# Optimization experiments

Measured on AMD Instinct MI355X. Metric: run time of the kernel, lower is better.

Reference implementation:

```python
import jax, jax.numpy as jnp
import numpy as np

B, S, D, L = 32, 1024, 768, 12

def setup_inputs() -> dict:
    key = jax.random.key(0)
    ks = jax.random.split(key, 10)
    hidden_states = jax.random.normal(ks[0], (B, S, D), dtype=jnp.float32)
    Wq = jax.random.normal(ks[1], (L, D, D), dtype=jnp.float32) * 0.02
    Wk = jax.random.normal(ks[2], (L, D, D), dtype=jnp.float32) * 0.02
    Wv = jax.random.normal(ks[3], (L, D, D), dtype=jnp.float32) * 0.02
    bq = jnp.zeros((L, D), dtype=jnp.float32)
    bk = jnp.zeros((L, D), dtype=jnp.float32)
    bv = jnp.zeros((L, D), dtype=jnp.float32)
    l_k = jnp.full((L, D), 0.8, dtype=jnp.float32)  # iA3 scales, init 0.8 per source
    l_v = jnp.full((L, D), 0.8, dtype=jnp.float32)
    W_head = jax.random.normal(ks[4], (D, 1), dtype=jnp.float32) * 0.02
    b_head = jnp.zeros((1,), dtype=jnp.float32)
    return {"hidden_states": hidden_states, "Wq": Wq, "bq": bq, "Wk": Wk, "bk": bk,
            "Wv": Wv, "bv": bv, "l_k": l_k, "l_v": l_v, "W_head": W_head, "b_head": b_head}

def reference(hidden_states, Wq, bq, Wk, bk, Wv, bv, l_k, l_v, W_head, b_head):
    scale = 1.0 / jnp.sqrt(jnp.float32(D))

    def layer_step(h, params):
        wq, bq_i, wk, bk_i, wv, bv_i, lk, lv = params
        Q = jnp.einsum('bsd,de->bse', h, wq) + bq_i
        K = (jnp.einsum('bsd,de->bse', h, wk) + bk_i) * lk  # iA3 per-channel scale on K
        V = (jnp.einsum('bsd,de->bse', h, wv) + bv_i) * lv  # iA3 per-channel scale on V
        attn = jax.nn.softmax(jnp.einsum('bqd,bkd->bqk', Q, K) * scale, axis=-1)
        h_new = jnp.einsum('bqk,bkd->bqd', attn, V)  # note: no residual/LN, matches source
        return h_new, None

    h, _ = jax.lax.scan(layer_step, hidden_states, (Wq, bq, Wk, bk, Wv, bv, l_k, l_v))
    pooled = h[:, 0, :]  # CLS token
    out = pooled @ W_head + b_head  # [B, 1]
    return out[:, 0]
```

## Files before the change

kernel.cpp:

```cpp
#include <hip/hip_runtime.h>
#include <hip/hip_fp16.h>
#include <math.h>

#define B_ 32
#define S_ 1024
#define D_ 768
#define L_ 12
#define SD 786432LL
#define SS 1048576LL
#define DD 589824LL
#define LDL 1769472LL

typedef _Float16 half8 __attribute__((ext_vector_type(8)));
typedef float f32x4 __attribute__((ext_vector_type(4)));
typedef unsigned short u16;

#define SW(lr) ((((lr) ^ ((lr) >> 3)) & 7))

__global__ __launch_bounds__(256, 2)
void gemm_qkv_k(const __half* __restrict__ A, const __half* __restrict__ Wt,
                const float* __restrict__ biasC, const float* __restrict__ scaleC,
                float aBias,
                __half* __restrict__ CQ, __half* __restrict__ CK, __half* __restrict__ CVt,
                int nBase, int tilesX, int mPerXcd)
{
    __shared__ __align__(16) u16 smem[16384];
    const int K = 768;

    const int flat = blockIdx.x;
    const int xcd = flat & 7;
    const int jj = flat >> 3;
    const int mLocal = jj / tilesX;
    const int nxI = jj - mLocal * tilesX;
    const int n0 = nxI * 128;
    const int m0 = (xcd * mPerXcd + mLocal) * 128;

    const int t = threadIdx.x;
    const int l = t & 63, w = t >> 6;
    const int wm = (w & 1) * 64, wn = (w >> 1) * 64;

    const int u0 = t, u1 = t + 256;
    const int r0 = u0 >> 2, c0 = (u0 & 3) ^ (r0 & 3);
    const int r1 = u1 >> 2, c1 = (u1 & 3) ^ (r1 & 3);
    const __half* gA0 = A + (long long)(m0 + r0) * K + c0 * 8;
    const __half* gA1 = A + (long long)(m0 + r1) * K + c1 * 8;
    const __half* gB0 = Wt + (long long)(n0 + r0) * K + c0 * 8;
    const __half* gB1 = Wt + (long long)(n0 + r1) * K + c1 * 8;
    u16* lA0 = &smem[u0 * 8];
    u16* lA1 = &smem[u1 * 8];
    u16* lB0 = &smem[4096 + u0 * 8];
    u16* lB1 = &smem[4096 + u1 * 8];

    int aoff[4], boff[4];
    const int kc = l >> 4;
    #pragma unroll
    for (int mt = 0; mt < 4; ++mt) {
        int rr = wm + mt * 16 + (l & 15);
        aoff[mt] = (rr * 4 + (kc ^ (rr & 3))) * 8;
        int rb = wn + mt * 16 + (l & 15);
        boff[mt] = (rb * 4 + (kc ^ (rb & 3))) * 8;
    }

    f32x4 acc[4][4];
    #pragma unroll
    for (int i = 0; i < 4; ++i)
        #pragma unroll
        for (int j = 0; j < 4; ++j)
            acc[i][j] = (f32x4){0.f, 0.f, 0.f, 0.f};

    for (int k0 = 0; k0 < K; k0 += 32) {
        __builtin_amdgcn_global_load_lds((const __attribute__((address_space(1))) void*)(gA0 + k0),
                                         (__attribute__((address_space(3))) void*)lA0, 16, 0, 0);
        __builtin_amdgcn_global_load_lds((const __attribute__((address_space(1))) void*)(gA1 + k0),
                                         (__attribute__((address_space(3))) void*)lA1, 16, 0, 0);
        __builtin_amdgcn_global_load_lds((const __attribute__((address_space(1))) void*)(gB0 + k0),
                                         (__attribute__((address_space(3))) void*)lB0, 16, 0, 0);
        __builtin_amdgcn_global_load_lds((const __attribute__((address_space(1))) void*)(gB1 + k0),
                                         (__attribute__((address_space(3))) void*)lB1, 16, 0, 0);
        __syncthreads();

        half8 af[4], bf[4];
        #pragma unroll
        for (int mt = 0; mt < 4; ++mt) af[mt] = *(const half8*)(const void*)&smem[aoff[mt]];
        #pragma unroll
        for (int nt = 0; nt < 4; ++nt) bf[nt] = *(const half8*)(const void*)&smem[4096 + boff[nt]];

        #pragma unroll
        for (int nt = 0; nt < 4; ++nt)
            #pragma unroll
            for (int mt = 0; mt < 4; ++mt)
                acc[mt][nt] = __builtin_amdgcn_mfma_f32_16x16x32_f16(af[mt], bf[nt], acc[mt][nt], 0, 0, 0);
        __syncthreads();
    }

    const int nCat0 = n0 + nBase;
    const int region = nCat0 / 768;
    const int colBase = nCat0 - region * 768;

    float badd[4], bmul[4];
    #pragma unroll
    for (int nt = 0; nt < 4; ++nt) {
        int gn = nCat0 + wn + nt * 16 + (l & 15);
        badd[nt] = aBias * biasC[gn];
        bmul[nt] = scaleC[gn];
    }

    const int qbase = w * 4096;
    #pragma unroll
    for (int mt = 0; mt < 4; ++mt) {
        #pragma unroll
        for (int nt = 0; nt < 4; ++nt) {
            #pragma unroll
            for (int i = 0; i < 4; ++i) {
                int lrow = mt * 16 + ((l >> 4) << 2) + i;
                int lcol = nt * 16 + (l & 15);
                float v = (acc[mt][nt][i] + badd[nt]) * bmul[nt];
                int cc = lcol >> 3, c7 = lcol & 7;
                smem[qbase + lrow * 64 + ((cc ^ SW(lrow)) << 3) + c7] =
                    __half_as_ushort(__float2half(v));
            }
        }
    }
    __syncthreads();

    if (region < 2) {
        __half* Creg = region ? CK : CQ;
        #pragma unroll
        for (int p = 0; p < 8; ++p) {
            int u = t + p * 256;
            int R = u >> 4, cc = u & 15;
            int qb = ((R >> 6) + ((cc >> 3) << 1)) * 4096;
            int lr = R & 63, lcc = cc & 7;
            half8 val = *(const half8*)(const void*)&smem[qb + lr * 64 + ((lcc ^ SW(lr)) << 3)];
            *(half8*)(void*)&Creg[(long long)(m0 + R) * 768 + colBase + cc * 8] = val;
        }
    } else {
        #pragma unroll
        for (int p = 0; p < 8; ++p) {
            int u = t + p * 256;
            int Crow = u >> 4, mcc = u & 15;
            __align__(16) u16 tmp[8];
            #pragma unroll
            for (int j = 0; j < 8; ++j) {
                int m = mcc * 8 + j;
                int qb = ((m >> 6) + ((Crow >> 6) << 1)) * 4096;
                int lr = m & 63, lcol = Crow & 63;
                int lcc = lcol >> 3;
                tmp[j] = smem[qb + lr * 64 + ((lcc ^ SW(lr)) << 3) + (lcol & 7)];
            }
            long long b = m0 >> 10;
            __half* dst = CVt + b * SD + (long long)(colBase + Crow) * 1024 + (m0 & 1023) + mcc * 8;
            *(half8*)(void*)dst = *(const half8*)(const void*)tmp;
        }
    }
}

template<int SWIZ, int MODE>
__global__ __launch_bounds__(256, 2)
void gemm_att_k(const __half* __restrict__ A, const __half* __restrict__ B,
                float aAcc, __half* __restrict__ C, int K, int ldc,
                long long sA, long long sB, long long sC,
                int tilesX, int tilesPB, int bpx,
                float* __restrict__ rsp, const float* __restrict__ invsum)
{
    __shared__ __align__(16) u16 smem[16384];
    __shared__ float sums[128 * 17];

    int nxI, ny;
    long long bz;
    if (SWIZ) {
        int flat = blockIdx.x;
        int xcd = flat & 7;
        int j = flat >> 3;
        int bLocal = j / tilesPB;
        int tt = j - bLocal * tilesPB;
        bz = (long long)(xcd * bpx + bLocal);
        ny = tt / tilesX;
        nxI = tt - ny * tilesX;
    } else {
        nxI = blockIdx.x; ny = blockIdx.y; bz = blockIdx.z;
    }

    const int t = threadIdx.x;
    const int l = t & 63, w = t >> 6;
    const int n0 = nxI * 128;
    const int m0 = ny * 128;
    A += bz * sA; B += bz * sB; C += bz * sC;

    const int wm = (w & 1) * 64, wn = (w >> 1) * 64;

    const int u0 = t, u1 = t + 256;
    const int r0 = u0 >> 2, c0 = (u0 & 3) ^ (r0 & 3);
    const int r1 = u1 >> 2, c1 = (u1 & 3) ^ (r1 & 3);
    const __half* gA0 = A + (long long)(m0 + r0) * K + c0 * 8;
    const __half* gA1 = A + (long long)(m0 + r1) * K + c1 * 8;
    const __half* gB0 = B + (long long)(n0 + r0) * K + c0 * 8;
    const __half* gB1 = B + (long long)(n0 + r1) * K + c1 * 8;
    u16* lA0 = &smem[u0 * 8];
    u16* lA1 = &smem[u1 * 8];
    u16* lB0 = &smem[4096 + u0 * 8];
    u16* lB1 = &smem[4096 + u1 * 8];

    int aoff[4], boff[4];
    const int kc = l >> 4;
    #pragma unroll
    for (int mt = 0; mt < 4; ++mt) {
        int rr = wm + mt * 16 + (l & 15);
        aoff[mt] = (rr * 4 + (kc ^ (rr & 3))) * 8;
        int rb = wn + mt * 16 + (l & 15);
        boff[mt] = (rb * 4 + (kc ^ (rb & 3))) * 8;
    }

    f32x4 acc[4][4];
    #pragma unroll
    for (int i = 0; i < 4; ++i)
        #pragma unroll
        for (int j = 0; j < 4; ++j)
            acc[i][j] = (f32x4){0.f, 0.f, 0.f, 0.f};

    for (int k0 = 0; k0 < K; k0 += 32) {
        __builtin_amdgcn_global_load_lds((const __attribute__((address_space(1))) void*)(gA0 + k0),
                                         (__attribute__((address_space(3))) void*)lA0, 16, 0, 0);
        __builtin_amdgcn_global_load_lds((const __attribute__((address_space(1))) void*)(gA1 + k0),
                                         (__attribute__((address_space(3))) void*)lA1, 16, 0, 0);
        __builtin_amdgcn_global_load_lds((const __attribute__((address_space(1))) void*)(gB0 + k0),
                                         (__attribute__((address_space(3))) void*)lB0, 16, 0, 0);
        __builtin_amdgcn_global_load_lds((const __attribute__((address_space(1))) void*)(gB1 + k0),
                                         (__attribute__((address_space(3))) void*)lB1, 16, 0, 0);
        __syncthreads();

        half8 af[4], bf[4];
        #pragma unroll
        for (int mt = 0; mt < 4; ++mt) af[mt] = *(const half8*)(const void*)&smem[aoff[mt]];
        #pragma unroll
        for (int nt = 0; nt < 4; ++nt) bf[nt] = *(const half8*)(const void*)&smem[4096 + boff[nt]];

        #pragma unroll
        for (int nt = 0; nt < 4; ++nt)
            #pragma unroll
            for (int mt = 0; mt < 4; ++mt)
                acc[mt][nt] = __builtin_amdgcn_mfma_f32_16x16x32_f16(af[mt], bf[nt], acc[mt][nt], 0, 0, 0);
        __syncthreads();
    }

    float invr[4][4];
    if (MODE == 2) {
        #pragma unroll
        for (int mt = 0; mt < 4; ++mt)
            #pragma unroll
            for (int i = 0; i < 4; ++i)
                invr[mt][i] = invsum[bz * 1024 + m0 + wm + mt * 16 + ((l >> 4) << 2) + i];
    }

    const int qbase = w * 4096;
    #pragma unroll
    for (int mt = 0; mt < 4; ++mt) {
        #pragma unroll
        for (int nt = 0; nt < 4; ++nt) {
            #pragma unroll
            for (int i = 0; i < 4; ++i) {
                int lrow = mt * 16 + ((l >> 4) << 2) + i;
                int lcol = nt * 16 + (l & 15);
                float v;
                if (MODE == 1)      v = __expf(acc[mt][nt][i] * aAcc);
                else                v = acc[mt][nt][i] * aAcc * invr[mt][i];
                int cc = lcol >> 3, c7 = lcol & 7;
                smem[qbase + lrow * 64 + ((cc ^ SW(lrow)) << 3) + c7] =
                    __half_as_ushort(__float2half(v));
            }
        }
    }
    __syncthreads();

    #pragma unroll
    for (int p = 0; p < 8; ++p) {
        int u = t + p * 256;
        int R = u >> 4, cc = u & 15;
        int qb = ((R >> 6) + ((cc >> 3) << 1)) * 4096;
        int lr = R & 63, lcc = cc & 7;
        half8 val = *(const half8*)(const void*)&smem[qb + lr * 64 + ((lcc ^ SW(lr)) << 3)];
        *(half8*)(void*)&C[(long long)(m0 + R) * ldc + n0 + cc * 8] = val;
        if (MODE == 1) {
            float s8 = 0.f;
            #pragma unroll
            for (int j = 0; j < 8; ++j) s8 += (float)val[j];
            sums[R * 17 + cc] = s8;
        }
    }
    if (MODE == 1) {
        __syncthreads();
        if (t < 128) {
            float s = 0.f;
            #pragma unroll
            for (int c = 0; c < 16; ++c) s += sums[t * 17 + c];
            rsp[bz * 8192 + (long long)(m0 + t) * 8 + nxI] = s;
        }
    }
}

__global__ __launch_bounds__(256)
void rowsuminv_k(const float* __restrict__ rsp, float* __restrict__ inv, int n)
{
    int i = blockIdx.x * 256 + threadIdx.x;
    if (i < n) {
        const float* p = rsp + (long long)i * 8;
        float s = ((p[0] + p[1]) + (p[2] + p[3])) + ((p[4] + p[5]) + (p[6] + p[7]));
        inv[i] = 1.0f / s;
    }
}

__global__ __launch_bounds__(256)
void cvt32to16_k(const float* __restrict__ X, __half* __restrict__ Y)
{
    long long i = ((long long)blockIdx.x * 256 + threadIdx.x) * 4;
    float4 v = *(const float4*)&X[i];
    *(__half2*)&Y[i]     = __floats2half2_rn(v.x, v.y);
    *(__half2*)&Y[i + 2] = __floats2half2_rn(v.z, v.w);
}

__global__ __launch_bounds__(256)
void wtrans_k(const float* __restrict__ W, __half* __restrict__ Wt,
              long long ldL, int rowOff)
{
    __shared__ float Ls[64][65];
    const int lyr = blockIdx.z;
    const int k0 = blockIdx.y * 64, n0 = blockIdx.x * 64;
    const float* src = W + (long long)lyr * DD;
    __half* dst = Wt + (long long)lyr * ldL;
    const int t = threadIdx.x;
    #pragma unroll
    for (int p = 0; p < 4; ++p) {
        int u = t + p * 256;
        int r = u >> 4, c4 = (u & 15) * 4;
        float4 v = *(const float4*)&src[(long long)(k0 + r) * D_ + n0 + c4];
        Ls[r][c4] = v.x; Ls[r][c4 + 1] = v.y; Ls[r][c4 + 2] = v.z; Ls[r][c4 + 3] = v.w;
    }
    __syncthreads();
    #pragma unroll
    for (int p = 0; p < 2; ++p) {
        int u = t + p * 256;
        int n = u >> 3, kc8 = (u & 7) * 8;
        __align__(16) u16 tmp[8];
        #pragma unroll
        for (int j = 0; j < 8; ++j) {
            _Float16 h = (_Float16)Ls[kc8 + j][n];
            tmp[j] = *(const u16*)&h;
        }
        *(half8*)(void*)&dst[(long long)(rowOff + n0 + n) * D_ + k0 + kc8] =
            *(const half8*)(const void*)tmp;
    }
}

__global__ __launch_bounds__(256)
void bscat_k(const float* __restrict__ bq, const float* __restrict__ bk,
             const float* __restrict__ bv, const float* __restrict__ lk,
             const float* __restrict__ lv, float* __restrict__ bsb,
             float* __restrict__ bss)
{
    int i = blockIdx.x * 256 + threadIdx.x;
    if (i >= L_ * 2304) return;
    int l = i / 2304, p = i - l * 2304;
    int r = p / 768, c = p - r * 768;
    float b, s;
    if (r == 0)      { b = bq[l * 768 + c]; s = 1.f; }
    else if (r == 1) { b = bk[l * 768 + c]; s = lk[l * 768 + c]; }
    else             { b = bv[l * 768 + c]; s = lv[l * 768 + c]; }
    bsb[i] = b; bss[i] = s;
}

__global__ __launch_bounds__(256)
void q0_k(const __half* __restrict__ H16, const __half* __restrict__ Wcat,
          const float* __restrict__ bq, float* __restrict__ q0f, float sig)
{
    const int b = blockIdx.x;
    const int n = blockIdx.y * 256 + threadIdx.x;
    const int t = threadIdx.x;
    __shared__ __half hrow[768];
    const __half* h = H16 + (long long)b * SD;
    hrow[t] = h[t]; hrow[t + 256] = h[t + 256]; hrow[t + 512] = h[t + 512];
    __syncthreads();
    const __half* wr = Wcat + 11LL * LDL + (long long)n * 768;
    float acc = 0.f;
    for (int k = 0; k < 768; ++k) acc += (float)hrow[k] * (float)wr[k];
    q0f[b * 768 + n] = acc + sig * bq[11 * 768 + n];
}

__global__ __launch_bounds__(256)
void s0_k(const float* __restrict__ q0f, const __half* __restrict__ K16,
          float* __restrict__ s0f, int b0, float aQK)
{
    const int z = blockIdx.x;
    const int b = b0 + z;
    const int s = blockIdx.y * 256 + threadIdx.x;
    const int t = threadIdx.x;
    __shared__ float qrow[768];
    qrow[t] = q0f[b * 768 + t];
    qrow[t + 256] = q0f[b * 768 + t + 256];
    qrow[t + 512] = q0f[b * 768 + t + 512];
    __syncthreads();
    const __half* kr = K16 + (long long)z * SD + (long long)s * 768;
    float acc = 0.f;
    for (int k = 0; k < 768; ++k) acc += qrow[k] * (float)kr[k];
    s0f[b * 1024 + s] = acc * aQK;
}

__global__ __launch_bounds__(256)
void sm0_k(float* __restrict__ s0f, int b0)
{
    float* p = s0f + (long long)(b0 + blockIdx.x) * 1024;
    const int t = threadIdx.x;
    float v[4];
    float mx = -1e30f;
    #pragma unroll
    for (int j = 0; j < 4; ++j) { v[j] = p[t + 256 * j]; mx = fmaxf(mx, v[j]); }
    __shared__ float red[256];
    red[t] = mx; __syncthreads();
    for (int s = 128; s > 0; s >>= 1) { if (t < s) red[t] = fmaxf(red[t], red[t + s]); __syncthreads(); }
    mx = red[0];
    __syncthreads();
    float sum = 0.f;
    #pragma unroll
    for (int j = 0; j < 4; ++j) { v[j] = __expf(v[j] - mx); sum += v[j]; }
    red[t] = sum; __syncthreads();
    for (int s = 128; s > 0; s >>= 1) { if (t < s) red[t] += red[t + s]; __syncthreads(); }
    const float inv = 1.0f / red[0];
    __syncthreads();
    #pragma unroll
    for (int j = 0; j < 4; ++j) p[t + 256 * j] = v[j] * inv;
}

__global__ __launch_bounds__(256)
void o0_k(const float* __restrict__ p0f, const __half* __restrict__ Vt16,
          float* __restrict__ o0f, int b0, float invSig)
{
    const int z = blockIdx.x;
    const int b = b0 + z;
    const int d = blockIdx.y * 256 + threadIdx.x;
    const int t = threadIdx.x;
    __shared__ float prow[1024];
    #pragma unroll
    for (int j = 0; j < 4; ++j) prow[t + 256 * j] = p0f[b * 1024 + t + 256 * j];
    __syncthreads();
    const __half* vr = Vt16 + (long long)z * SD + (long long)d * 1024;
    float acc = 0.f;
    for (int s = 0; s < 1024; ++s) acc += prow[s] * (float)vr[s];
    o0f[b * 768 + d] = acc * invSig;
}

__global__ __launch_bounds__(256)
void headf_k(const float* __restrict__ o0f, const float* __restrict__ Wh,
             const float* __restrict__ bh, float* __restrict__ out)
{
    const int b = blockIdx.x;
    const int t = threadIdx.x;
    float s = 0.f;
    for (int d = t; d < 768; d += 256) s += o0f[b * 768 + d] * Wh[d];
    __shared__ float red[256];
    red[t] = s; __syncthreads();
    for (int k = 128; k > 0; k >>= 1) { if (t < k) red[t] += red[t + k]; __syncthreads(); }
    if (t == 0) out[b] = red[0] + bh[0];
}

extern "C" void kernel_launch(void* const* d_in, const int* in_sizes, int n_in,
                              void* d_out, int out_size, void* d_ws, size_t ws_size,
                              hipStream_t stream)
{
    const float* hs = (const float*)d_in[0];
    const float* Wq = (const float*)d_in[1];
    const float* bq = (const float*)d_in[2];
    const float* Wk = (const float*)d_in[3];
    const float* bk = (const float*)d_in[4];
    const float* Wv = (const float*)d_in[5];
    const float* bv = (const float*)d_in[6];
    const float* lk = (const float*)d_in[7];
    const float* lv = (const float*)d_in[8];
    const float* Wh = (const float*)d_in[9];
    const float* bh = (const float*)d_in[10];
    float* outp = (float*)d_out;

    __half* H16  = (__half*)d_ws;
    __half* Wcat = H16 + (long long)B_ * SD;
    float*  bsb  = (float*)(Wcat + 12LL * LDL);
    float*  bss  = bsb + 12 * 2304;
    float*  q0f  = bss + 12 * 2304;
    float*  s0f  = q0f + 32 * 768;
    float*  o0f  = s0f + 32 * 1024;
    float*  rsp  = o0f + 32 * 768;
    float*  inv  = rsp + 32LL * 8192;
    __half* Q16  = (__half*)(inv + 32 * 1024);

    const size_t baseBytes = (size_t)((char*)Q16 - (char*)d_ws);
    const size_t perG = ((size_t)(3 * SD) + (size_t)SS) * 2;
    long long avail = (long long)ws_size - (long long)baseBytes;
    int G = (avail > 0) ? (int)(avail / perG) : 1;
    if (G >= 32) G = 32; else if (G >= 16) G = 16; else if (G >= 8) G = 8;
    if (G < 1) G = 1;
    __half* K16  = Q16 + (long long)G * SD;
    __half* Vt16 = K16 + (long long)G * SD;
    __half* P16  = Vt16 + (long long)G * SD;

    cvt32to16_k<<<dim3((int)((B_ * SD) / 1024)), 256, 0, stream>>>(hs, H16);
    wtrans_k<<<dim3(12, 12, 12), 256, 0, stream>>>(Wq, Wcat, LDL, 0);
    wtrans_k<<<dim3(12, 12, 12), 256, 0, stream>>>(Wk, Wcat, LDL, 768);
    wtrans_k<<<dim3(12, 12, 12), 256, 0, stream>>>(Wv, Wcat, LDL, 1536);
    bscat_k<<<dim3((L_ * 2304 + 255) / 256), 256, 0, stream>>>(bq, bk, bv, lk, lv, bsb, bss);

    const float scq = 0.036084391824351615f;
    float sig = 1.f;

    for (int lyr = 0; lyr < L_ - 1; ++lyr) {
        const __half* W = Wcat + (long long)lyr * LDL;
        const float* bb = bsb + lyr * 2304;
        const float* ss = bss + lyr * 2304;
        const float aQK = scq / (sig * sig);

        for (int b0 = 0; b0 < B_; b0 += G) {
            const int nb = (B_ - b0 < G) ? (B_ - b0) : G;
            const __half* hg = H16 + (long long)b0 * SD;

            gemm_qkv_k<<<dim3(18 * 8 * nb), 256, 0, stream>>>(
                hg, W, bb, ss, sig, Q16, K16, Vt16, 0, 18, nb);

            if ((nb & 7) == 0) {
                gemm_att_k<1, 1><<<dim3(nb * 64), 256, 0, stream>>>(
                    Q16, K16, aQK, P16, 768, 1024, SD, SD, SS, 8, 64, nb >> 3, rsp, nullptr);
            } else {
                gemm_att_k<0, 1><<<dim3(8, 8, nb), 256, 0, stream>>>(
                    Q16, K16, aQK, P16, 768, 1024, SD, SD, SS, 8, 64, 1, rsp, nullptr);
            }

            rowsuminv_k<<<dim3(nb * 4), 256, 0, stream>>>(rsp, inv, nb * 1024);

            if ((nb & 7) == 0) {
                gemm_att_k<1, 2><<<dim3(nb * 48), 256, 0, stream>>>(
                    P16, Vt16, 4.f, H16 + (long long)b0 * SD, 1024, 768, SS, SD, SD,
                    6, 48, nb >> 3, nullptr, inv);
            } else {
                gemm_att_k<0, 2><<<dim3(6, 8, nb), 256, 0, stream>>>(
                    P16, Vt16, 4.f, H16 + (long long)b0 * SD, 1024, 768, SS, SD, SD,
                    6, 48, 1, nullptr, inv);
            }
        }
        sig *= 4.f;
    }

    const float aQK = scq / (sig * sig);
    q0_k<<<dim3(B_, 3), 256, 0, stream>>>(H16, Wcat, bq, q0f, sig);

    for (int b0 = 0; b0 < B_; b0 += G) {
        const int nb = (B_ - b0 < G) ? (B_ - b0) : G;
        const __half* hg = H16 + (long long)b0 * SD;

        gemm_qkv_k<<<dim3(12 * 8 * nb), 256, 0, stream>>>(
            hg, Wcat + 11LL * LDL + 768LL * 768, bsb + 11 * 2304, bss + 11 * 2304,
            sig, K16 , K16, Vt16, 768, 12, nb);

        s0_k<<<dim3(nb, 4), 256, 0, stream>>>(q0f, K16, s0f, b0, aQK);
        sm0_k<<<dim3(nb), 256, 0, stream>>>(s0f, b0);
        o0_k<<<dim3(nb, 3), 256, 0, stream>>>(s0f, Vt16, o0f, b0, 1.f / sig);
    }

    headf_k<<<dim3(B_), 256, 0, stream>>>(o0f, Wh, bh, outp);
}
```

Baseline: 3.572 ms.

## Swap MFMA operands for packed epilogue stores and fuse row-sum inverse

Swaps the A/B operands of the MFMA so each lane holds four consecutive columns of one row. The epilogue can then convert them to half2 pairs and write 8-byte packed LDS stores under a new XOR swizzle, replacing per-element 2-byte stores. It also removes the separate rowsuminv kernel: the PV GEMM now sums the 8 partial row sums itself and divides once per row. Each PV block redoes the partial-sum reduction, which costs a few extra global loads in exchange for one fewer launch per batch group.

```diff
diff --git a/kernel.cpp b/kernel.cpp
--- a/kernel.cpp
+++ b/kernel.cpp
@@ -15,7 +15,6 @@
 typedef float f32x4 __attribute__((ext_vector_type(4)));
 typedef unsigned short u16;
 
-#define SW(lr) ((((lr) ^ ((lr) >> 3)) & 7))
 
 __global__ __launch_bounds__(256, 2)
 void gemm_qkv_k(const __half* __restrict__ A, const __half* __restrict__ Wt,
@@ -37,6 +36,7 @@
 
     const int t = threadIdx.x;
     const int l = t & 63, w = t >> 6;
+    const int quad = l >> 4;
     const int wm = (w & 1) * 64, wn = (w >> 1) * 64;
 
     const int u0 = t, u1 = t + 256;
@@ -89,7 +89,7 @@
         for (int nt = 0; nt < 4; ++nt)
             #pragma unroll
             for (int mt = 0; mt < 4; ++mt)
-                acc[mt][nt] = __builtin_amdgcn_mfma_f32_16x16x32_f16(af[mt], bf[nt], acc[mt][nt], 0, 0, 0);
+                acc[mt][nt] = __builtin_amdgcn_mfma_f32_16x16x32_f16(bf[nt], af[mt], acc[mt][nt], 0, 0, 0);
         __syncthreads();
     }
 
@@ -97,28 +97,30 @@
     const int region = nCat0 / 768;
     const int colBase = nCat0 - region * 768;
 
-    float badd[4], bmul[4];
+    const int qbase = w * 4096;
     #pragma unroll
     for (int nt = 0; nt < 4; ++nt) {
-        int gn = nCat0 + wn + nt * 16 + (l & 15);
-        badd[nt] = aBias * biasC[gn];
-        bmul[nt] = scaleC[gn];
-    }
-
-    const int qbase = w * 4096;
-    #pragma unroll
-    for (int mt = 0; mt < 4; ++mt) {
-        #pragma unroll
-        for (int nt = 0; nt < 4; ++nt) {
-            #pragma unroll
-            for (int i = 0; i < 4; ++i) {
-                int lrow = mt * 16 + ((l >> 4) << 2) + i;
-                int lcol = nt * 16 + (l & 15);
-                float v = (acc[mt][nt][i] + badd[nt]) * bmul[nt];
-                int cc = lcol >> 3, c7 = lcol & 7;
-                smem[qbase + lrow * 64 + ((cc ^ SW(lrow)) << 3) + c7] =
-                    __half_as_ushort(__float2half(v));
-            }
+        float badd[4], bmul[4];
+        #pragma unroll
+        for (int i = 0; i < 4; ++i) {
+            int gn = nCat0 + wn + nt * 16 + quad * 4 + i;
+            badd[i] = aBias * biasC[gn];
+            bmul[i] = scaleC[gn];
+        }
+        #pragma unroll
+        for (int mt = 0; mt < 4; ++mt) {
+            int lr = mt * 16 + (l & 15);
+            float v0 = (acc[mt][nt][0] + badd[0]) * bmul[0];
+            float v1 = (acc[mt][nt][1] + badd[1]) * bmul[1];
+            float v2 = (acc[mt][nt][2] + badd[2]) * bmul[2];
+            float v3 = (acc[mt][nt][3] + badd[3]) * bmul[3];
+            __half2 h01 = __floats2half2_rn(v0, v1);
+            __half2 h23 = __floats2half2_rn(v2, v3);
+            uint2 pk;
+            pk.x = *(const unsigned int*)&h01;
+            pk.y = *(const unsigned int*)&h23;
+            int pos = qbase + lr * 64 + (((nt ^ (lr & 3))) << 4) + (quad << 2);
+            *(uint2*)(void*)&smem[pos] = pk;
         }
     }
     __syncthreads();
@@ -130,8 +132,9 @@
             int u = t + p * 256;
             int R = u >> 4, cc = u & 15;
             int qb = ((R >> 6) + ((cc >> 3) << 1)) * 4096;
-            int lr = R & 63, lcc = cc & 7;
-            half8 val = *(const half8*)(const void*)&smem[qb + lr * 64 + ((lcc ^ SW(lr)) << 3)];
+            int lr = R & 63, hc = cc & 7;
+            int pos = qb + lr * 64 + (((hc >> 1) ^ (lr & 3)) << 4) + ((hc & 1) << 3);
+            half8 val = *(const half8*)(const void*)&smem[pos];
             *(half8*)(void*)&Creg[(long long)(m0 + R) * 768 + colBase + cc * 8] = val;
         }
     } else {
@@ -140,13 +143,14 @@
             int u = t + p * 256;
             int Crow = u >> 4, mcc = u & 15;
             __align__(16) u16 tmp[8];
+            int lc = Crow & 63;
             #pragma unroll
             for (int j = 0; j < 8; ++j) {
                 int m = mcc * 8 + j;
                 int qb = ((m >> 6) + ((Crow >> 6) << 1)) * 4096;
-                int lr = m & 63, lcol = Crow & 63;
-                int lcc = lcol >> 3;
-                tmp[j] = smem[qb + lr * 64 + ((lcc ^ SW(lr)) << 3) + (lcol & 7)];
+                int lr = m & 63;
+                int pos = qb + lr * 64 + (((lc >> 4) ^ (lr & 3)) << 4) + (lc & 15);
+                tmp[j] = smem[pos];
             }
             long long b = m0 >> 10;
             __half* dst = CVt + b * SD + (long long)(colBase + Crow) * 1024 + (m0 & 1023) + mcc * 8;
@@ -160,8 +164,7 @@
 void gemm_att_k(const __half* __restrict__ A, const __half* __restrict__ B,
                 float aAcc, __half* __restrict__ C, int K, int ldc,
                 long long sA, long long sB, long long sC,
-                int tilesX, int tilesPB, int bpx,
-                float* __restrict__ rsp, const float* __restrict__ invsum)
+                int tilesX, int tilesPB, int bpx, float* __restrict__ rsp)
 {
     __shared__ __align__(16) u16 smem[16384];
     __shared__ float sums[128 * 17];
@@ -183,6 +186,7 @@
 
     const int t = threadIdx.x;
     const int l = t & 63, w = t >> 6;
+    const int quad = l >> 4;
     const int n0 = nxI * 128;
     const int m0 = ny * 128;
     A += bz * sA; B += bz * sB; C += bz * sC;
@@ -239,35 +243,41 @@
         for (int nt = 0; nt < 4; ++nt)
             #pragma unroll
             for (int mt = 0; mt < 4; ++mt)
-                acc[mt][nt] = __builtin_amdgcn_mfma_f32_16x16x32_f16(af[mt], bf[nt], acc[mt][nt], 0, 0, 0);
+                acc[mt][nt] = __builtin_amdgcn_mfma_f32_16x16x32_f16(bf[nt], af[mt], acc[mt][nt], 0, 0, 0);
         __syncthreads();
     }
 
-    float invr[4][4];
-    if (MODE == 2) {
-        #pragma unroll
-        for (int mt = 0; mt < 4; ++mt)
-            #pragma unroll
-            for (int i = 0; i < 4; ++i)
-                invr[mt][i] = invsum[bz * 1024 + m0 + wm + mt * 16 + ((l >> 4) << 2) + i];
-    }
-
     const int qbase = w * 4096;
     #pragma unroll
     for (int mt = 0; mt < 4; ++mt) {
+        int lr = mt * 16 + (l & 15);
+        float scl = aAcc;
+        if (MODE == 2) {
+            const float* pr = rsp + bz * 8192 + (long long)(m0 + wm + lr) * 8;
+            float s = ((pr[0] + pr[1]) + (pr[2] + pr[3])) + ((pr[4] + pr[5]) + (pr[6] + pr[7]));
+            scl = aAcc / s;
+        }
         #pragma unroll
         for (int nt = 0; nt < 4; ++nt) {
-            #pragma unroll
-            for (int i = 0; i < 4; ++i) {
-                int lrow = mt * 16 + ((l >> 4) << 2) + i;
-                int lcol = nt * 16 + (l & 15);
-                float v;
-                if (MODE == 1)      v = __expf(acc[mt][nt][i] * aAcc);
-                else                v = acc[mt][nt][i] * aAcc * invr[mt][i];
-                int cc = lcol >> 3, c7 = lcol & 7;
-                smem[qbase + lrow * 64 + ((cc ^ SW(lrow)) << 3) + c7] =
-                    __half_as_ushort(__float2half(v));
+            float v0, v1, v2, v3;
+            if (MODE == 1) {
+                v0 = __expf(acc[mt][nt][0] * aAcc);
+                v1 = __expf(acc[mt][nt][1] * aAcc);
+                v2 = __expf(acc[mt][nt][2] * aAcc);
+                v3 = __expf(acc[mt][nt][3] * aAcc);
+            } else {
+                v0 = acc[mt][nt][0] * scl;
+                v1 = acc[mt][nt][1] * scl;
+                v2 = acc[mt][nt][2] * scl;
+                v3 = acc[mt][nt][3] * scl;
             }
+            __half2 h01 = __floats2half2_rn(v0, v1);
+            __half2 h23 = __floats2half2_rn(v2, v3);
+            uint2 pk;
+            pk.x = *(const unsigned int*)&h01;
+            pk.y = *(const unsigned int*)&h23;
+            int pos = qbase + lr * 64 + (((nt ^ (lr & 3))) << 4) + (quad << 2);
+            *(uint2*)(void*)&smem[pos] = pk;
         }
     }
     __syncthreads();
@@ -277,8 +287,9 @@
         int u = t + p * 256;
         int R = u >> 4, cc = u & 15;
         int qb = ((R >> 6) + ((cc >> 3) << 1)) * 4096;
-        int lr = R & 63, lcc = cc & 7;
-        half8 val = *(const half8*)(const void*)&smem[qb + lr * 64 + ((lcc ^ SW(lr)) << 3)];
+        int lr = R & 63, hc = cc & 7;
+        int pos = qb + lr * 64 + (((hc >> 1) ^ (lr & 3)) << 4) + ((hc & 1) << 3);
+        half8 val = *(const half8*)(const void*)&smem[pos];
         *(half8*)(void*)&C[(long long)(m0 + R) * ldc + n0 + cc * 8] = val;
         if (MODE == 1) {
             float s8 = 0.f;
@@ -295,17 +306,6 @@
             for (int c = 0; c < 16; ++c) s += sums[t * 17 + c];
             rsp[bz * 8192 + (long long)(m0 + t) * 8 + nxI] = s;
         }
-    }
-}
-
-__global__ __launch_bounds__(256)
-void rowsuminv_k(const float* __restrict__ rsp, float* __restrict__ inv, int n)
-{
-    int i = blockIdx.x * 256 + threadIdx.x;
-    if (i < n) {
-        const float* p = rsp + (long long)i * 8;
-        float s = ((p[0] + p[1]) + (p[2] + p[3])) + ((p[4] + p[5]) + (p[6] + p[7]));
-        inv[i] = 1.0f / s;
     }
 }
 
@@ -486,8 +486,7 @@
     float*  s0f  = q0f + 32 * 768;
     float*  o0f  = s0f + 32 * 1024;
     float*  rsp  = o0f + 32 * 768;
-    float*  inv  = rsp + 32LL * 8192;
-    __half* Q16  = (__half*)(inv + 32 * 1024);
+    __half* Q16  = (__half*)(rsp + 32LL * 8192);
 
     const size_t baseBytes = (size_t)((char*)Q16 - (char*)d_ws);
     const size_t perG = ((size_t)(3 * SD) + (size_t)SS) * 2;
@@ -523,22 +522,20 @@
 
             if ((nb & 7) == 0) {
                 gemm_att_k<1, 1><<<dim3(nb * 64), 256, 0, stream>>>(
-                    Q16, K16, aQK, P16, 768, 1024, SD, SD, SS, 8, 64, nb >> 3, rsp, nullptr);
+                    Q16, K16, aQK, P16, 768, 1024, SD, SD, SS, 8, 64, nb >> 3, rsp);
             } else {
                 gemm_att_k<0, 1><<<dim3(8, 8, nb), 256, 0, stream>>>(
-                    Q16, K16, aQK, P16, 768, 1024, SD, SD, SS, 8, 64, 1, rsp, nullptr);
+                    Q16, K16, aQK, P16, 768, 1024, SD, SD, SS, 8, 64, 1, rsp);
             }
-
-            rowsuminv_k<<<dim3(nb * 4), 256, 0, stream>>>(rsp, inv, nb * 1024);
 
             if ((nb & 7) == 0) {
                 gemm_att_k<1, 2><<<dim3(nb * 48), 256, 0, stream>>>(
                     P16, Vt16, 4.f, H16 + (long long)b0 * SD, 1024, 768, SS, SD, SD,
-                    6, 48, nb >> 3, nullptr, inv);
+                    6, 48, nb >> 3, rsp);
             } else {
                 gemm_att_k<0, 2><<<dim3(6, 8, nb), 256, 0, stream>>>(
                     P16, Vt16, 4.f, H16 + (long long)b0 * SD, 1024, 768, SS, SD, SD,
-                    6, 48, 1, nullptr, inv);
+                    6, 48, 1, rsp);
             }
         }
         sig *= 4.f;
```

Measured after the change: 3.859 ms. +8.0%, slower.
